# Performance work log

Measured on AMD Instinct MI355X. Metric: run time of the kernel, lower is better.

The kernel has to match this reference:

```python
import jax, jax.numpy as jnp
import numpy as np


def setup_inputs() -> dict:
    key = jax.random.key(0)
    k1, k2, k3, k4, k5 = jax.random.split(key, 5)
    B, S, E2, D = 32, 2048, 1024, 512
    return {
        "output_encoder": jax.random.normal(k1, (B, S, E2), dtype=jnp.float32),
        "last_hidden_decoder": jax.random.normal(k2, (B, D), dtype=jnp.float32),
        "W_att": jax.random.normal(k3, (E2 + D, D), dtype=jnp.float32) * 0.02,
        "b_att": jax.random.normal(k4, (D,), dtype=jnp.float32) * 0.02,
        "v": jax.random.normal(k5, (D,), dtype=jnp.float32) * 0.02,
    }


def reference(output_encoder, last_hidden_decoder, W_att, b_att, v):
    # output_encoder: (B, S, E2); last_hidden_decoder: (B, D)
    B, S, E2 = output_encoder.shape
    D = last_hidden_decoder.shape[-1]
    # Split W_att to avoid materializing the repeated+concat tensor:
    # concat(enc, dec) @ W == enc @ W_enc + dec @ W_dec  (dec broadcast over seq)
    W_enc, W_dec = W_att[:E2], W_att[E2:]
    dec_proj = last_hidden_decoder @ W_dec  # (B, D)
    energy = jnp.tanh(jnp.einsum("bse,ed->bsd", output_encoder, W_enc)
                      + dec_proj[:, None, :] + b_att)  # (B, S, D)
    attention = jnp.einsum("bsd,d->bs", energy, v)  # (B, S)
    attention_weights = jax.nn.softmax(attention, axis=1)  # (B, S)
    # context: (B, 1, E2)
    context = jnp.einsum("bs,bse->be", attention_weights, output_encoder)[:, None, :]
    return context
```

## Files before the change

kernel.cpp:

```cpp
#include <hip/hip_runtime.h>
#include <stdint.h>


typedef __attribute__((ext_vector_type(8))) __bf16 bf16x8;
typedef __attribute__((ext_vector_type(4))) float f32x4;

__device__ __forceinline__ uint16_t f32_to_bf16_rne(float f) {
  union { float f; uint32_t u; } v; v.f = f;
  uint32_t u = v.u;
  return (uint16_t)((u + 0x7FFFu + ((u >> 16) & 1u)) >> 16);
}

__device__ __forceinline__ float tanh_fast(float x) {
  float e = __expf(2.0f * x);
  return 1.0f - 2.0f * __builtin_amdgcn_rcpf(e + 1.0f);
}

__global__ __launch_bounds__(256) void prep_kernel(
    const float* __restrict__ dec,
    const float* __restrict__ Watt,
    const float* __restrict__ batt,
    float* __restrict__ cbias,
    uint16_t* __restrict__ Wb,
    float* __restrict__ out)
{
  const int t = blockIdx.x * 256 + threadIdx.x;

  for (int i = t; i < 32768; i += 16384) out[i] = 0.0f;

  {
    const int b = t >> 9, d = t & 511;
    const float* wd = Watt + 1024 * 512 + d;
    const float* dv = dec + b * 512;
    float s0 = 0.f, s1 = 0.f, s2 = 0.f, s3 = 0.f;
    #pragma unroll 4
    for (int k = 0; k < 512; k += 4) {
      s0 += dv[k + 0] * wd[(k + 0) * 512];
      s1 += dv[k + 1] * wd[(k + 1) * 512];
      s2 += dv[k + 2] * wd[(k + 2) * 512];
      s3 += dv[k + 3] * wd[(k + 3) * 512];
    }
    cbias[t] = batt[d] + ((s0 + s1) + (s2 + s3));
  }

  uint4* WbV = (uint4*)Wb;
  #pragma unroll
  for (int i = 0; i < 4; ++i) {
    const int u   = t + 16384 * i;
    const int c   = u >> 11;
    const int rem = u & 2047;
    const int wn  = rem >> 8;
    const int nf  = (rem >> 6) & 3;
    const int ln  = rem & 63;
    const int kb  = c * 32 + ((ln >> 4) << 3);
    const int d   = wn * 64 + nf * 16 + (ln & 15);
    uint32_t h[8];
    #pragma unroll
    for (int kk = 0; kk < 8; ++kk) {
      float f = Watt[(size_t)(kb + kk) * 512 + d];
      h[kk] = f32_to_bf16_rne(f);
    }
    uint4 val;
    val.x = h[0] | (h[1] << 16);
    val.y = h[2] | (h[3] << 16);
    val.z = h[4] | (h[5] << 16);
    val.w = h[6] | (h[7] << 16);
    WbV[u] = val;
  }
}

__global__ __launch_bounds__(512, 4) void energy_kernel(
    const float* __restrict__ x,
    const uint16_t* __restrict__ Wb,
    const float* __restrict__ cbias,
    const float* __restrict__ vvec,
    float* __restrict__ att)
{
  __shared__ __align__(16) uint8_t AL[2][64 * 64];

  const int tid  = threadIdx.x;
  const int lane = tid & 63;
  const int wave = tid >> 6;
  const int l15  = lane & 15;
  const int l4   = lane >> 4;
  const int brow0 = blockIdx.x * 64;
  const int b     = brow0 >> 11;

  const int r_st = tid >> 3, q_st = tid & 7;
  const int aoff = r_st * 64 + ((q_st * 8) ^ (((r_st >> 1) & 3) << 4));
  const float* asrc = x + (size_t)(brow0 + r_st) * 1024 + q_st * 4;
  const uint8_t* wslice = (const uint8_t*)Wb + (size_t)wave * 4096 + (size_t)lane * 16;

  f32x4 acc[4][4];
  #pragma unroll
  for (int mf = 0; mf < 4; ++mf)
    #pragma unroll
    for (int nf = 0; nf < 4; ++nf)
      acc[mf][nf] = (f32x4){0.f, 0.f, 0.f, 0.f};

  float4 av_cur = *(const float4*)(asrc);
  bf16x8 bA[4], bB[4];
  {
    const bf16x8* bs = (const bf16x8*)(wslice);
    bA[0] = bs[0]; bA[1] = bs[64]; bA[2] = bs[128]; bA[3] = bs[192];
  }

#define CHUNK(C, BCUR, BNXT)                                                   \
  {                                                                            \
    const int c_ = (C);                                                        \
    uint8_t* Ab = AL[c_ & 1];                                                  \
    uint32_t lo_ = (uint32_t)f32_to_bf16_rne(av_cur.x) |                       \
                   ((uint32_t)f32_to_bf16_rne(av_cur.y) << 16);                \
    uint32_t hi_ = (uint32_t)f32_to_bf16_rne(av_cur.z) |                       \
                   ((uint32_t)f32_to_bf16_rne(av_cur.w) << 16);                \
    *(uint2*)(Ab + aoff) = make_uint2(lo_, hi_);                               \
    const int cn_ = (c_ < 31) ? c_ + 1 : 31;                                   \
    av_cur = *(const float4*)(asrc + cn_ * 32);                                \
    asm volatile("s_waitcnt lgkmcnt(0)" ::: "memory");                         \
    __builtin_amdgcn_s_barrier();                                              \
    asm volatile("" ::: "memory");                                             \
    {                                                                          \
      const bf16x8* bs_ = (const bf16x8*)(wslice + (size_t)cn_ * 32768);       \
      BNXT[0] = bs_[0]; BNXT[1] = bs_[64];                                     \
      BNXT[2] = bs_[128]; BNXT[3] = bs_[192];                                  \
    }                                                                          \
    _Pragma("unroll")                                                          \
    for (int mf = 0; mf < 4; ++mf) {                                           \
      const int r_ = mf * 16 + l15;                                            \
      bf16x8 afm = *(const bf16x8*)(Ab + r_ * 64 +                             \
                                    ((l4 * 16) ^ (((r_ >> 1) & 3) << 4)));     \
      acc[mf][0] = __builtin_amdgcn_mfma_f32_16x16x32_bf16(afm, BCUR[0], acc[mf][0], 0, 0, 0); \
      acc[mf][1] = __builtin_amdgcn_mfma_f32_16x16x32_bf16(afm, BCUR[1], acc[mf][1], 0, 0, 0); \
      acc[mf][2] = __builtin_amdgcn_mfma_f32_16x16x32_bf16(afm, BCUR[2], acc[mf][2], 0, 0, 0); \
      acc[mf][3] = __builtin_amdgcn_mfma_f32_16x16x32_bf16(afm, BCUR[3], acc[mf][3], 0, 0, 0); \
    }                                                                          \
  }

  for (int c = 0; c < 32; c += 2) {
    CHUNK(c, bA, bB);
    CHUNK(c + 1, bB, bA);
  }
#undef CHUNK

  float cb[4], vv[4];
  #pragma unroll
  for (int nf = 0; nf < 4; ++nf) {
    const int d = wave * 64 + nf * 16 + l15;
    cb[nf] = cbias[b * 512 + d];
    vv[nf] = vvec[d];
  }

  __syncthreads();
  float* red = (float*)AL;
  if (tid < 64) red[tid] = 0.0f;
  __syncthreads();

  #pragma unroll
  for (int mf = 0; mf < 4; ++mf) {
    float s[4] = {0.f, 0.f, 0.f, 0.f};
    #pragma unroll
    for (int nf = 0; nf < 4; ++nf) {
      #pragma unroll
      for (int j = 0; j < 4; ++j) {
        const float e = acc[mf][nf][j] + cb[nf];
        s[j] += tanh_fast(e) * vv[nf];
      }
    }
    #pragma unroll
    for (int j = 0; j < 4; ++j) {
      float r = s[j];
      r += __shfl_xor(r, 1);
      r += __shfl_xor(r, 2);
      r += __shfl_xor(r, 4);
      r += __shfl_xor(r, 8);
      if (l15 == 0) atomicAdd(&red[mf * 16 + 4 * l4 + j], r);
    }
  }
  __syncthreads();
  if (tid < 64) att[brow0 + tid] = red[tid];
}

__global__ __launch_bounds__(256) void softmax_kernel(float* __restrict__ att) {
  const int b = blockIdx.x;
  float* row = att + b * 2048;
  const int tid = threadIdx.x;
  __shared__ float redm[4], reds[4];

  float vals[8];
  float m = -1e30f;
  #pragma unroll
  for (int i = 0; i < 8; ++i) { vals[i] = row[tid + 256 * i]; m = fmaxf(m, vals[i]); }
  #pragma unroll
  for (int msk = 1; msk < 64; msk <<= 1) m = fmaxf(m, __shfl_xor(m, msk));
  if ((tid & 63) == 0) redm[tid >> 6] = m;
  __syncthreads();
  m = fmaxf(fmaxf(redm[0], redm[1]), fmaxf(redm[2], redm[3]));

  float s = 0.f;
  #pragma unroll
  for (int i = 0; i < 8; ++i) { vals[i] = __expf(vals[i] - m); s += vals[i]; }
  #pragma unroll
  for (int msk = 1; msk < 64; msk <<= 1) s += __shfl_xor(s, msk);
  if ((tid & 63) == 0) reds[tid >> 6] = s;
  __syncthreads();
  const float inv = 1.0f / (((reds[0] + reds[1]) + (reds[2] + reds[3])));
  #pragma unroll
  for (int i = 0; i < 8; ++i) row[tid + 256 * i] = vals[i] * inv;
}

__global__ __launch_bounds__(256) void context_kernel(
    const float* __restrict__ x,
    const float* __restrict__ w,
    float* __restrict__ out)
{
  const int blk = blockIdx.x;
  const int b = blk >> 4, sc = blk & 15;
  const int tid = threadIdx.x;
  const float* xb = x + ((size_t)(b * 2048 + sc * 128)) * 1024 + tid * 4;
  const float* wb = w + b * 2048 + sc * 128;

  float4 acc = {0.f, 0.f, 0.f, 0.f};
  for (int si = 0; si < 128; ++si) {
    const float ww = wb[si];
    const float4 xv = *(const float4*)(xb + (size_t)si * 1024);
    acc.x += ww * xv.x;
    acc.y += ww * xv.y;
    acc.z += ww * xv.z;
    acc.w += ww * xv.w;
  }
  float* o = out + b * 1024 + tid * 4;
  atomicAdd(o + 0, acc.x);
  atomicAdd(o + 1, acc.y);
  atomicAdd(o + 2, acc.z);
  atomicAdd(o + 3, acc.w);
}

extern "C" void kernel_launch(void* const* d_in, const int* in_sizes, int n_in,
                              void* d_out, int out_size, void* d_ws, size_t ws_size,
                              hipStream_t stream) {
  const float* x    = (const float*)d_in[0];
  const float* dec  = (const float*)d_in[1];
  const float* Watt = (const float*)d_in[2];
  const float* batt = (const float*)d_in[3];
  const float* v    = (const float*)d_in[4];
  float* out = (float*)d_out;

  uint8_t* ws = (uint8_t*)d_ws;
  float*    att   = (float*)ws;
  float*    cbias = (float*)(ws + 256 * 1024);
  uint16_t* Wb    = (uint16_t*)(ws + 320 * 1024);

  prep_kernel<<<64, 256, 0, stream>>>(dec, Watt, batt, cbias, Wb, out);
  energy_kernel<<<1024, 512, 0, stream>>>(x, Wb, cbias, v, att);
  softmax_kernel<<<32, 256, 0, stream>>>(att);
  context_kernel<<<512, 256, 0, stream>>>(x, att, out);
}
```

Measured before the change: 143.8 us.

## Double energy kernel M-tile to 128 rows to halve weight reloads

Each energy block now processes 128 encoder rows instead of 64, doubling the accumulator tile so every W_enc fragment loaded from global memory feeds twice as many MFMAs. The grid is halved and launch bounds drop to 2 blocks per CU to make room for the extra registers. Encoder loads also switch to nontemporal loads to reduce cache pollution. This trades lower occupancy and higher register pressure for less weight traffic.

Measured after the change: 139.4 us. 1.03x faster.

```diff
diff --git a/kernel.cpp b/kernel.cpp
--- a/kernel.cpp
+++ b/kernel.cpp
@@ -69,36 +69,40 @@
   }
 }
 
-__global__ __launch_bounds__(512, 4) void energy_kernel(
+__global__ __launch_bounds__(512, 2) void energy_kernel(
     const float* __restrict__ x,
     const uint16_t* __restrict__ Wb,
     const float* __restrict__ cbias,
     const float* __restrict__ vvec,
     float* __restrict__ att)
 {
-  __shared__ __align__(16) uint8_t AL[2][64 * 64];
+  __shared__ __align__(16) uint8_t AL[2][128 * 64];
 
   const int tid  = threadIdx.x;
   const int lane = tid & 63;
   const int wave = tid >> 6;
   const int l15  = lane & 15;
   const int l4   = lane >> 4;
-  const int brow0 = blockIdx.x * 64;
+  const int brow0 = blockIdx.x * 128;
   const int b     = brow0 >> 11;
 
   const int r_st = tid >> 3, q_st = tid & 7;
-  const int aoff = r_st * 64 + ((q_st * 8) ^ (((r_st >> 1) & 3) << 4));
-  const float* asrc = x + (size_t)(brow0 + r_st) * 1024 + q_st * 4;
+  const int swz  = ((r_st >> 1) & 3) << 4;
+  const int aoff0 = r_st * 64 + ((q_st * 8) ^ swz);
+  const int aoff1 = (r_st + 64) * 64 + ((q_st * 8) ^ swz);
+  const float* asrc0 = x + (size_t)(brow0 + r_st) * 1024 + q_st * 4;
+  const float* asrc1 = x + (size_t)(brow0 + r_st + 64) * 1024 + q_st * 4;
   const uint8_t* wslice = (const uint8_t*)Wb + (size_t)wave * 4096 + (size_t)lane * 16;
 
-  f32x4 acc[4][4];
-  #pragma unroll
-  for (int mf = 0; mf < 4; ++mf)
+  f32x4 acc[8][4];
+  #pragma unroll
+  for (int mf = 0; mf < 8; ++mf)
     #pragma unroll
     for (int nf = 0; nf < 4; ++nf)
       acc[mf][nf] = (f32x4){0.f, 0.f, 0.f, 0.f};
 
-  float4 av_cur = *(const float4*)(asrc);
+  f32x4 av0 = __builtin_nontemporal_load((const f32x4*)(asrc0));
+  f32x4 av1 = __builtin_nontemporal_load((const f32x4*)(asrc1));
   bf16x8 bA[4], bB[4];
   {
     const bf16x8* bs = (const bf16x8*)(wslice);
@@ -109,23 +113,31 @@
   {                                                                            \
     const int c_ = (C);                                                        \
     uint8_t* Ab = AL[c_ & 1];                                                  \
-    uint32_t lo_ = (uint32_t)f32_to_bf16_rne(av_cur.x) |                       \
-                   ((uint32_t)f32_to_bf16_rne(av_cur.y) << 16);                \
-    uint32_t hi_ = (uint32_t)f32_to_bf16_rne(av_cur.z) |                       \
-                   ((uint32_t)f32_to_bf16_rne(av_cur.w) << 16);                \
-    *(uint2*)(Ab + aoff) = make_uint2(lo_, hi_);                               \
-    const int cn_ = (c_ < 31) ? c_ + 1 : 31;                                   \
-    av_cur = *(const float4*)(asrc + cn_ * 32);                                \
+    {                                                                          \
+      uint32_t lo = (uint32_t)f32_to_bf16_rne(av0.x) |                         \
+                    ((uint32_t)f32_to_bf16_rne(av0.y) << 16);                  \
+      uint32_t hi = (uint32_t)f32_to_bf16_rne(av0.z) |                         \
+                    ((uint32_t)f32_to_bf16_rne(av0.w) << 16);                  \
+      *(uint2*)(Ab + aoff0) = make_uint2(lo, hi);                              \
+      lo = (uint32_t)f32_to_bf16_rne(av1.x) |                                  \
+           ((uint32_t)f32_to_bf16_rne(av1.y) << 16);                           \
+      hi = (uint32_t)f32_to_bf16_rne(av1.z) |                                  \
+           ((uint32_t)f32_to_bf16_rne(av1.w) << 16);                           \
+      *(uint2*)(Ab + aoff1) = make_uint2(lo, hi);                              \
+    }                                                                          \
+    const int cn_ = (c_ + 1 < 32) ? c_ + 1 : 31;                               \
+    av0 = __builtin_nontemporal_load((const f32x4*)(asrc0 + cn_ * 32));        \
+    av1 = __builtin_nontemporal_load((const f32x4*)(asrc1 + cn_ * 32));        \
     asm volatile("s_waitcnt lgkmcnt(0)" ::: "memory");                         \
     __builtin_amdgcn_s_barrier();                                              \
     asm volatile("" ::: "memory");                                             \
     {                                                                          \
       const bf16x8* bs_ = (const bf16x8*)(wslice + (size_t)cn_ * 32768);       \
-      BNXT[0] = bs_[0]; BNXT[1] = bs_[64];                                     \
+      BNXT[0] = bs_[0];   BNXT[1] = bs_[64];                                   \
       BNXT[2] = bs_[128]; BNXT[3] = bs_[192];                                  \
     }                                                                          \
     _Pragma("unroll")                                                          \
-    for (int mf = 0; mf < 4; ++mf) {                                           \
+    for (int mf = 0; mf < 8; ++mf) {                                           \
       const int r_ = mf * 16 + l15;                                            \
       bf16x8 afm = *(const bf16x8*)(Ab + r_ * 64 +                             \
                                     ((l4 * 16) ^ (((r_ >> 1) & 3) << 4)));     \
@@ -152,11 +164,11 @@
 
   __syncthreads();
   float* red = (float*)AL;
-  if (tid < 64) red[tid] = 0.0f;
-  __syncthreads();
-
-  #pragma unroll
-  for (int mf = 0; mf < 4; ++mf) {
+  if (tid < 128) red[tid] = 0.0f;
+  __syncthreads();
+
+  #pragma unroll
+  for (int mf = 0; mf < 8; ++mf) {
     float s[4] = {0.f, 0.f, 0.f, 0.f};
     #pragma unroll
     for (int nf = 0; nf < 4; ++nf) {
@@ -177,7 +189,7 @@
     }
   }
   __syncthreads();
-  if (tid < 64) att[brow0 + tid] = red[tid];
+  if (tid < 128) att[brow0 + tid] = red[tid];
 }
 
 __global__ __launch_bounds__(256) void softmax_kernel(float* __restrict__ att) {
@@ -251,7 +263,7 @@
   uint16_t* Wb    = (uint16_t*)(ws + 320 * 1024);
 
   prep_kernel<<<64, 256, 0, stream>>>(dec, Watt, batt, cbias, Wb, out);
-  energy_kernel<<<1024, 512, 0, stream>>>(x, Wb, cbias, v, att);
+  energy_kernel<<<512, 512, 0, stream>>>(x, Wb, cbias, v, att);
   softmax_kernel<<<32, 256, 0, stream>>>(att);
   context_kernel<<<512, 256, 0, stream>>>(x, att, out);
 }
```
